# Optimization experiments

Measured on AMD Instinct MI355X. Metric: run time of the kernel, lower is better.

Reference implementation:

```python
import jax, jax.numpy as jnp
import numpy as np

B, T, C, H, HS, L, V = 16, 2048, 16, 2, 8, 2, 256
EPS = 1e-5


def _ln(x, g, b):
    m = jnp.mean(x, axis=-1, keepdims=True)
    v = jnp.mean((x - m) ** 2, axis=-1, keepdims=True)
    return (x - m) / jnp.sqrt(v + EPS) * g + b


def setup_inputs() -> dict:
    key = jax.random.key(0)
    ks = jax.random.split(key, 10)
    p = lambda k, s: (0.02 * jax.random.normal(k, s)).astype(jnp.float32)
    return {
        "idx": jax.random.randint(ks[0], (B, T), 0, V),
        "tok_emb": p(ks[1], (V, C)),          # tied with lm_head
        "pos_emb": p(ks[2], (T, C)),
        "wq": p(ks[3], (L, H, C, HS)),
        "wk": p(ks[4], (L, H, C, HS)),
        "wv": p(ks[5], (L, H, C, HS)),
        "wo": p(ks[6], (L, C, C)),            # torch Linear weight: (out, in)
        "ln1_g": jnp.ones((L, C), jnp.float32),
        "ln1_b": jnp.zeros((L, C), jnp.float32),
        "ln2_g": jnp.ones((L, C), jnp.float32),
        "ln2_b": jnp.zeros((L, C), jnp.float32),
        "w1": p(ks[7], (L, 4 * C, C)),
        "w2": p(ks[8], (L, C, 4 * C)),
        "lnf_g": jnp.ones((C,), jnp.float32),
        "lnf_b": jnp.zeros((C,), jnp.float32),
    }


def reference(idx, tok_emb, pos_emb, wq, wk, wv, wo, ln1_g, ln1_b,
              ln2_g, ln2_b, w1, w2, lnf_g, lnf_b):
    Tc = idx.shape[1]
    x = tok_emb[idx] + pos_emb[:Tc]                      # [B,T,C]
    causal = jnp.tril(jnp.ones((Tc, Tc), dtype=bool))
    scale = HS ** -0.5
    for l in range(L):
        h = _ln(x, ln1_g[l], ln1_b[l])
        q = jnp.einsum('btc,hcs->bhts', h, wq[l])
        k = jnp.einsum('btc,hcs->bhts', h, wk[l])
        v = jnp.einsum('btc,hcs->bhts', h, wv[l])
        scores = jnp.einsum('bhts,bhus->bhtu', q, k) * scale
        scores = jnp.where(causal, scores, -jnp.inf)
        attn = jax.nn.softmax(scores, axis=-1)           # [B,H,T,T]
        o = jnp.einsum('bhtu,bhus->bhts', attn, v)       # [B,H,T,HS]
        o = o.transpose(0, 2, 1, 3).reshape(x.shape[0], Tc, C)  # concat heads
        x = x + o @ wo[l].T
        h = _ln(x, ln2_g[l], ln2_b[l])
        x = x + jax.nn.relu(h @ w1[l].T) @ w2[l].T
    x = _ln(x, lnf_g, lnf_b)
    return x @ tok_emb.T                                 # tied lm_head: [B,T,V]
```

## Files before the change

kernel.cpp:

```cpp
#include <hip/hip_runtime.h>
#include <math.h>

constexpr int Bc  = 16;
constexpr int Tc  = 2048;
constexpr int Cc  = 16;
constexpr int Hc  = 2;
constexpr int HSc = 8;
constexpr int Vc  = 256;
constexpr int BT  = Bc * Tc;
constexpr float EPSc = 1e-5f;


typedef short s8v __attribute__((ext_vector_type(8)));
typedef float f4v __attribute__((ext_vector_type(4)));

constexpr int WS = 20;

__device__ inline float shx(float v, int m) { return __shfl_xor(v, m, 64); }

__device__ inline unsigned short f2bf(float f) {
  union { float f; unsigned u; } c; c.f = f;
  unsigned u = c.u + 0x7fffu + ((c.u >> 16) & 1u);
  return (unsigned short)(u >> 16);
}

__device__ inline unsigned cvtpk(float a, float b) {
  unsigned r;
  asm("v_cvt_pk_bf16_f32 %0, %1, %2" : "=v"(r) : "v"(a), "v"(b));
  return r;
}

__device__ inline void layernorm16(const float* xr, float* h,
                                   const float* g, const float* b) {
  float m = 0.f;
#pragma unroll
  for (int c = 0; c < Cc; c++) m += xr[c];
  m *= (1.f / Cc);
  float var = 0.f;
#pragma unroll
  for (int c = 0; c < Cc; c++) { float d = xr[c] - m; var += d * d; }
  var *= (1.f / Cc);
  float rs = rsqrtf(var + EPSc);
#pragma unroll
  for (int c = 0; c < Cc; c++) h[c] = (xr[c] - m) * rs * g[c] + b[c];
}

__device__ inline void qkv_store_bf16(const float* h, const float* swq,
                                      const float* swk, const float* swv,
                                      int bb, int tt, int j,
                                      unsigned short* __restrict__ qb,
                                      unsigned short* __restrict__ kb,
                                      unsigned short* sv) {
  const float pre = 0.35355339059327373f * 1.4426950408889634f;
  int a = tt & 31;
  int col = (tt & 32) | ((((a & 15) >> 2)) << 3) | (((a >> 4) & 1) << 2) |
            (a & 3);
#pragma unroll
  for (int hh = 0; hh < Hc; hh++) {
    float q0 = 0.f, q1 = 0.f, k0 = 0.f, k1 = 0.f, v0 = 0.f, v1 = 0.f;
#pragma unroll
    for (int c = 0; c < Cc; c++) {
      float hv = h[c];
      const float* wqp = swq + (hh * Cc + c) * HSc + 2 * j;
      const float* wkp = swk + (hh * Cc + c) * HSc + 2 * j;
      const float* wvp = swv + (hh * Cc + c) * HSc + 2 * j;
      q0 += hv * wqp[0]; q1 += hv * wqp[1];
      k0 += hv * wkp[0]; k1 += hv * wkp[1];
      v0 += hv * wvp[0]; v1 += hv * wvp[1];
    }
    int bh = bb * Hc + hh;
    long rowb = ((long)bh * Tc + tt) * 8 + 2 * j;
    unsigned qp = (unsigned)f2bf(q0 * pre) | ((unsigned)f2bf(q1 * pre) << 16);
    unsigned kp = (unsigned)f2bf(k0) | ((unsigned)f2bf(k1) << 16);
    *(unsigned*)(qb + rowb) = qp;
    *(unsigned*)(kb + rowb) = kp;
    sv[(hh * 8 + 2 * j) * 64 + col]     = f2bf(v0);
    sv[(hh * 8 + 2 * j + 1) * 64 + col] = f2bf(v1);
  }
}

__device__ inline void vt_writeout(const unsigned short* sv, int bb, int t0,
                                   int tid, unsigned short* __restrict__ vt) {
  int r  = tid >> 4;
  int cs = (tid & 15) * 4;
  int bh = bb * Hc + (r >> 3);
  int d  = r & 7;
  *(uint2*)(vt + ((long)bh * 8 + d) * Tc + t0 + cs) =
      *(const uint2*)(sv + r * 64 + cs);
}

__global__ __launch_bounds__(256, 4) void embed_ln_qkv_kernel(
    const int* __restrict__ idx, const float* __restrict__ tok,
    const float* __restrict__ pos,
    const float* __restrict__ wq, const float* __restrict__ wk,
    const float* __restrict__ wv,
    const float* __restrict__ g, const float* __restrict__ b,
    float* __restrict__ x, unsigned short* __restrict__ qb,
    unsigned short* __restrict__ kb, unsigned short* __restrict__ vt,
    unsigned short* __restrict__ zp) {
  __shared__ float swq[256], swk[256], swv[256], sg[Cc], sb[Cc];
  __shared__ unsigned short sv[16 * 64];
  int tid = threadIdx.x;
  if (blockIdx.x == 0 && tid < 16) ((unsigned*)zp)[tid] = 0u;
  swq[tid] = wq[tid];
  swk[tid] = wk[tid];
  swv[tid] = wv[tid];
  if (tid < Cc) { sg[tid] = g[tid]; sb[tid] = b[tid]; }
  __syncthreads();

  int tk = blockIdx.x * 64 + (tid >> 2);
  int j  = tid & 3;
  int tt = tk & (Tc - 1);
  int bb = tk >> 11;
  int id = idx[tk];
  float xr[Cc];
  const float4* te = (const float4*)(tok + id * Cc);
  const float4* pe = (const float4*)(pos + tt * Cc);
#pragma unroll
  for (int i = 0; i < 4; i++) {
    float4 a = te[i], p = pe[i];
    xr[4*i] = a.x + p.x; xr[4*i+1] = a.y + p.y;
    xr[4*i+2] = a.z + p.z; xr[4*i+3] = a.w + p.w;
  }
  ((float4*)(x + (long)tk * Cc))[j] =
      make_float4(xr[4*j], xr[4*j+1], xr[4*j+2], xr[4*j+3]);
  float h[Cc];
  layernorm16(xr, h, sg, sb);
  qkv_store_bf16(h, swq, swk, swv, bb, tt, j, qb, kb, sv);
  __syncthreads();
  vt_writeout(sv, bb, (blockIdx.x * 64) & (Tc - 1), tid, vt);
}

__device__ inline void attn_wave(const unsigned short* __restrict__ qb,
                                 const unsigned short* __restrict__ kb,
                                 const unsigned short* __restrict__ vt,
                                 const unsigned short* __restrict__ zp,
                                 int bh, int pairId, int lane, int wv_,
                                 float* so) {
  int lq = lane & 15;
  int g4 = (lane >> 4) << 2;
  bool real16 = lane < 16;
  bool real8  = lq < 8;
  bool md[4];
#pragma unroll
  for (int r = 0; r < 4; r++) md[r] = (g4 + r) <= lq;

  const f4v zf = {0.f, 0.f, 0.f, 0.f};

#pragma unroll 1
  for (int hf = 0; hf < 2; hf++) {
    int qt = hf ? (127 - pairId) : pairId;
    int q0 = qt << 4;
    int NB = (qt + 2) >> 1;

    s8v qf = *(real16 ? (const s8v*)(qb + ((long)bh * Tc + q0 + lq) * 8)
                      : (const s8v*)zp);
    const unsigned short* kp_ = real16 ? kb + ((long)bh * Tc + lq) * 8 : zp;
    long kts = real16 ? 128 : 0;
    const unsigned short* vp_ =
        real8 ? vt + ((long)bh * 8 + lq) * Tc + (g4 << 1) : zp;
    long vts = real8 ? 32 : 0;

    f4v oacc = zf;
    float lsum = 0.f;

    s8v kf0 = *(const s8v*)kp_;
    s8v kf1 = *(const s8v*)(kp_ + kts);
    kp_ += 2 * kts;
    s8v vf = *(const s8v*)vp_;
    vp_ += vts;

    for (int b = 0; b < NB - 1; b++) {
      s8v kn0 = *(const s8v*)kp_;
      s8v kn1 = *(const s8v*)(kp_ + kts);
      kp_ += 2 * kts;
      s8v vn = *(const s8v*)vp_;
      vp_ += vts;

      f4v st0 = __builtin_amdgcn_mfma_f32_16x16x32_bf16(kf0, qf, zf, 0, 0, 0);
      f4v st1 = __builtin_amdgcn_mfma_f32_16x16x32_bf16(kf1, qf, zf, 0, 0, 0);
      float p00 = __builtin_amdgcn_exp2f(st0[0]);
      float p01 = __builtin_amdgcn_exp2f(st0[1]);
      float p02 = __builtin_amdgcn_exp2f(st0[2]);
      float p03 = __builtin_amdgcn_exp2f(st0[3]);
      float p10 = __builtin_amdgcn_exp2f(st1[0]);
      float p11 = __builtin_amdgcn_exp2f(st1[1]);
      float p12 = __builtin_amdgcn_exp2f(st1[2]);
      float p13 = __builtin_amdgcn_exp2f(st1[3]);
      lsum += ((p00 + p01) + (p02 + p03)) + ((p10 + p11) + (p12 + p13));
      union { unsigned u[4]; s8v s; } pu;
      pu.u[0] = cvtpk(p00, p01);
      pu.u[1] = cvtpk(p02, p03);
      pu.u[2] = cvtpk(p10, p11);
      pu.u[3] = cvtpk(p12, p13);
      oacc = __builtin_amdgcn_mfma_f32_16x16x32_bf16(pu.s, vf, oacc, 0, 0, 0);
      kf0 = kn0; kf1 = kn1; vf = vn;
    }

    {
      f4v st0 = __builtin_amdgcn_mfma_f32_16x16x32_bf16(kf0, qf, zf, 0, 0, 0);
      float p0[4], p1[4];
#pragma unroll
      for (int r = 0; r < 4; r++) p0[r] = __builtin_amdgcn_exp2f(st0[r]);
      if (qt & 1) {
        f4v st1 =
            __builtin_amdgcn_mfma_f32_16x16x32_bf16(kf1, qf, zf, 0, 0, 0);
#pragma unroll
        for (int r = 0; r < 4; r++) {
          float e = __builtin_amdgcn_exp2f(st1[r]);
          p1[r] = md[r] ? e : 0.f;
        }
      } else {
#pragma unroll
        for (int r = 0; r < 4; r++) {
          p0[r] = md[r] ? p0[r] : 0.f;
          p1[r] = 0.f;
        }
      }
      lsum += ((p0[0] + p0[1]) + (p0[2] + p0[3])) +
              ((p1[0] + p1[1]) + (p1[2] + p1[3]));
      union { unsigned u[4]; s8v s; } pu;
      pu.u[0] = cvtpk(p0[0], p0[1]);
      pu.u[1] = cvtpk(p0[2], p0[3]);
      pu.u[2] = cvtpk(p1[0], p1[1]);
      pu.u[3] = cvtpk(p1[2], p1[3]);
      oacc = __builtin_amdgcn_mfma_f32_16x16x32_bf16(pu.s, vf, oacc, 0, 0, 0);
    }

    lsum += shx(lsum, 16);
    lsum += shx(lsum, 32);
    float inv = 1.0f / lsum;
    float invr[4];
#pragma unroll
    for (int r = 0; r < 4; r++) invr[r] = __shfl(inv, g4 + r, 64);
    if (real8) {
      float* ob = so + (hf * 16 + g4) * WS + wv_ * 8 + lq;
#pragma unroll
      for (int r = 0; r < 4; r++) ob[r * WS] = oacc[r] * invr[r];
    }
  }
}

__device__ inline void tail_core(
    const float* so, const float* swo, const float* sw1, const float* sw2t,
    const float* sg2, const float* sb2, int tl, int j, float* xr) {
  float orow[Cc];
  {
    const float4* op = (const float4*)(so + tl * WS);
    float4 a = op[0], b = op[1], c = op[2], d = op[3];
    orow[0]=a.x; orow[1]=a.y; orow[2]=a.z; orow[3]=a.w;
    orow[4]=b.x; orow[5]=b.y; orow[6]=b.z; orow[7]=b.w;
    orow[8]=c.x; orow[9]=c.y; orow[10]=c.z; orow[11]=c.w;
    orow[12]=d.x; orow[13]=d.y; orow[14]=d.z; orow[15]=d.w;
  }
  float xc[4];
#pragma unroll
  for (int qq = 0; qq < 4; qq++) {
    int c = 4 * j + qq;
    const float4* wr = (const float4*)(swo + c * WS);
    float4 wa = wr[0], wb = wr[1], wc = wr[2], wd = wr[3];
    float acc = xr[c]
      + orow[0]*wa.x + orow[1]*wa.y + orow[2]*wa.z + orow[3]*wa.w
      + orow[4]*wb.x + orow[5]*wb.y + orow[6]*wb.z + orow[7]*wb.w
      + orow[8]*wc.x + orow[9]*wc.y + orow[10]*wc.z + orow[11]*wc.w
      + orow[12]*wd.x + orow[13]*wd.y + orow[14]*wd.z + orow[15]*wd.w;
    xc[qq] = acc;
  }
  {
    float p[4];
#pragma unroll
    for (int qq = 0; qq < 4; qq++) p[qq] = shx(xc[qq], 1);
    bool lo = (j & 1) == 0;
    float a8[8], b8[8];
#pragma unroll
    for (int qq = 0; qq < 4; qq++) {
      a8[qq]     = lo ? xc[qq] : p[qq];
      a8[4 + qq] = lo ? p[qq] : xc[qq];
    }
#pragma unroll
    for (int s = 0; s < 8; s++) b8[s] = shx(a8[s], 2);
    bool lo2 = (j & 2) == 0;
#pragma unroll
    for (int s = 0; s < 8; s++) {
      xr[s]     = lo2 ? a8[s] : b8[s];
      xr[8 + s] = lo2 ? b8[s] : a8[s];
    }
  }
  float h[Cc];
  layernorm16(xr, h, sg2, sb2);
  float r[Cc];
#pragma unroll
  for (int c = 0; c < Cc; c++) r[c] = 0.f;
#pragma unroll
  for (int i = 0; i < 16; i++) {
    int jj = i * 4 + j;
    const float4* w1r = (const float4*)(sw1 + jj * WS);
    float4 wa = w1r[0], wb = w1r[1], wc = w1r[2], wd = w1r[3];
    float acc =
        h[0]*wa.x + h[1]*wa.y + h[2]*wa.z + h[3]*wa.w
      + h[4]*wb.x + h[5]*wb.y + h[6]*wb.z + h[7]*wb.w
      + h[8]*wc.x + h[9]*wc.y + h[10]*wc.z + h[11]*wc.w
      + h[12]*wd.x + h[13]*wd.y + h[14]*wd.z + h[15]*wd.w;
    acc = fmaxf(acc, 0.f);
    const float4* w2r = (const float4*)(sw2t + jj * WS);
    float4 va = w2r[0], vb = w2r[1], vc = w2r[2], vd = w2r[3];
    r[0]+=acc*va.x;  r[1]+=acc*va.y;  r[2]+=acc*va.z;  r[3]+=acc*va.w;
    r[4]+=acc*vb.x;  r[5]+=acc*vb.y;  r[6]+=acc*vb.z;  r[7]+=acc*vb.w;
    r[8]+=acc*vc.x;  r[9]+=acc*vc.y;  r[10]+=acc*vc.z; r[11]+=acc*vc.w;
    r[12]+=acc*vd.x; r[13]+=acc*vd.y; r[14]+=acc*vd.z; r[15]+=acc*vd.w;
  }
#pragma unroll
  for (int c = 0; c < Cc; c++) r[c] += shx(r[c], 1);
#pragma unroll
  for (int c = 0; c < Cc; c++) r[c] += shx(r[c], 2);
#pragma unroll
  for (int c = 0; c < Cc; c++) xr[c] += r[c];
}

__global__ __launch_bounds__(128, 2) void attn_mid_kernel(
    const unsigned short* __restrict__ qb0,
    const unsigned short* __restrict__ kb0,
    const unsigned short* __restrict__ vt0,
    const unsigned short* __restrict__ zp,
    const float* __restrict__ wo, const float* __restrict__ g2,
    const float* __restrict__ b2, const float* __restrict__ w1,
    const float* __restrict__ w2,
    const float* __restrict__ wq, const float* __restrict__ wk,
    const float* __restrict__ wv, const float* __restrict__ g1,
    const float* __restrict__ b1,
    float* __restrict__ x, unsigned short* __restrict__ qb1,
    unsigned short* __restrict__ kb1, unsigned short* __restrict__ vt1) {
  __shared__ float swo[16 * WS], sw1[64 * WS], sw2t[64 * WS];
  __shared__ float swq[256], swk[256], swv[256];
  __shared__ float sg2[Cc], sb2[Cc], sg1[Cc], sb1[Cc];
  __shared__ float so[32 * WS];
  __shared__ unsigned short sv[2 * 16 * 16];
  int tid = threadIdx.x;
  for (int t = tid; t < 256; t += 128) {
    swq[t] = wq[t]; swk[t] = wk[t]; swv[t] = wv[t];
    swo[(t >> 4) * WS + (t & 15)] = wo[t];
  }
  for (int t = tid; t < 1024; t += 128) {
    sw1[(t >> 4) * WS + (t & 15)] = w1[t];
    sw2t[(t & 63) * WS + (t >> 6)] = w2[t];
  }
  if (tid < Cc) {
    sg2[tid] = g2[tid]; sb2[tid] = b2[tid];
    sg1[tid] = g1[tid]; sb1[tid] = b1[tid];
  }
  __syncthreads();

  int b  = blockIdx.x & 15;
  int p  = blockIdx.x >> 4;
  int wv_ = tid >> 6, lane = tid & 63;
  attn_wave(qb0, kb0, vt0, zp, b * Hc + wv_, p, lane, wv_, so);
  __syncthreads();

  int tl = tid >> 2, j = tid & 3;
  int qtT = (tl < 16) ? p : (127 - p);
  int tt  = qtT * 16 + (tl & 15);
  long tk = (long)b * Tc + tt;
  float xr[Cc];
  {
    const float4* xp = (const float4*)(x + tk * Cc);
#pragma unroll
    for (int i = 0; i < 4; i++) {
      float4 a = xp[i];
      xr[4*i]=a.x; xr[4*i+1]=a.y; xr[4*i+2]=a.z; xr[4*i+3]=a.w;
    }
  }
  tail_core(so, swo, sw1, sw2t, sg2, sb2, tl, j, xr);
  ((float4*)(x + tk * Cc))[j] =
      make_float4(xr[4*j], xr[4*j+1], xr[4*j+2], xr[4*j+3]);
  float h[Cc];
  layernorm16(xr, h, sg1, sb1);
  {
    const float pre = 0.35355339059327373f * 1.4426950408889634f;
    int i  = tt & 15;
    int cd = 4 * (i >> 2) + (i & 3);
    int tau = tl >> 4;
#pragma unroll
    for (int hh = 0; hh < Hc; hh++) {
      float q0 = 0.f, q1 = 0.f, k0 = 0.f, k1 = 0.f, v0 = 0.f, v1 = 0.f;
#pragma unroll
      for (int c = 0; c < Cc; c++) {
        float hv = h[c];
        const float* wqp = swq + (hh * Cc + c) * HSc + 2 * j;
        const float* wkp = swk + (hh * Cc + c) * HSc + 2 * j;
        const float* wvp = swv + (hh * Cc + c) * HSc + 2 * j;
        q0 += hv * wqp[0]; q1 += hv * wqp[1];
        k0 += hv * wkp[0]; k1 += hv * wkp[1];
        v0 += hv * wvp[0]; v1 += hv * wvp[1];
      }
      int bh = b * Hc + hh;
      long rowb = ((long)bh * Tc + tt) * 8 + 2 * j;
      *(unsigned*)(qb1 + rowb) =
          (unsigned)f2bf(q0 * pre) | ((unsigned)f2bf(q1 * pre) << 16);
      *(unsigned*)(kb1 + rowb) =
          (unsigned)f2bf(k0) | ((unsigned)f2bf(k1) << 16);
      sv[(tau * 16 + hh * 8 + 2 * j) * 16 + cd]     = f2bf(v0);
      sv[(tau * 16 + hh * 8 + 2 * j + 1) * 16 + cd] = f2bf(v1);
    }
  }
  __syncthreads();
  {
    int tau = tid >> 6, rr = (tid >> 2) & 15, G = tid & 3;
    int qt_ = tau ? (127 - p) : p;
    int bh  = b * Hc + (rr >> 3), d = rr & 7;
    int gcol = ((qt_ & ~1) << 4) + 8 * G + 4 * (qt_ & 1);
    *(uint2*)(vt1 + ((long)bh * 8 + d) * Tc + gcol) =
        *(const uint2*)(sv + (tau * 16 + rr) * 16 + 4 * G);
  }
}

__global__ __launch_bounds__(128, 2) void attn_lnf_head_kernel(
    const unsigned short* __restrict__ qb1,
    const unsigned short* __restrict__ kb1,
    const unsigned short* __restrict__ vt1,
    const unsigned short* __restrict__ zp,
    const float* __restrict__ wo, const float* __restrict__ g2,
    const float* __restrict__ b2, const float* __restrict__ w1,
    const float* __restrict__ w2, const float* __restrict__ gf,
    const float* __restrict__ bf,
    float* __restrict__ x, const float* __restrict__ tok,
    float* __restrict__ out) {
  __shared__ float swo[16 * WS], sw1[64 * WS], sw2t[64 * WS];
  __shared__ float sg2[Cc], sb2[Cc], sgf[Cc], sbf[Cc];
  __shared__ float so[32 * WS];
  __shared__ float shf[32 * WS];
  int tid = threadIdx.x;
  for (int t = tid; t < 256; t += 128) {
    swo[(t >> 4) * WS + (t & 15)] = wo[t];
  }
  for (int t = tid; t < 1024; t += 128) {
    sw1[(t >> 4) * WS + (t & 15)] = w1[t];
    sw2t[(t & 63) * WS + (t >> 6)] = w2[t];
  }
  if (tid < Cc) {
    sg2[tid] = g2[tid]; sb2[tid] = b2[tid];
    sgf[tid] = gf[tid]; sbf[tid] = bf[tid];
  }
  __syncthreads();

  int b  = blockIdx.x & 15;
  int p  = blockIdx.x >> 4;
  int wv_ = tid >> 6, lane = tid & 63;
  attn_wave(qb1, kb1, vt1, zp, b * Hc + wv_, p, lane, wv_, so);
  __syncthreads();

  int tl = tid >> 2, j = tid & 3;
  int qtT = (tl < 16) ? p : (127 - p);
  int tt  = qtT * 16 + (tl & 15);
  long tk = (long)b * Tc + tt;
  float xr[Cc];
  {
    const float4* xp = (const float4*)(x + tk * Cc);
#pragma unroll
    for (int i = 0; i < 4; i++) {
      float4 a = xp[i];
      xr[4*i]=a.x; xr[4*i+1]=a.y; xr[4*i+2]=a.z; xr[4*i+3]=a.w;
    }
  }
  tail_core(so, swo, sw1, sw2t, sg2, sb2, tl, j, xr);
  float h[Cc];
  layernorm16(xr, h, sgf, sbf);
  *(float4*)(shf + tl * WS + 4 * j) =
      make_float4(h[4*j], h[4*j+1], h[4*j+2], h[4*j+3]);
  __syncthreads();

  float4 e0a, e1a, e2a, e3a, e0b, e1b, e2b, e3b;
  {
    const float4* ea = (const float4*)(tok + tid * Cc);
    e0a = ea[0]; e1a = ea[1]; e2a = ea[2]; e3a = ea[3];
    const float4* eb = (const float4*)(tok + (tid + 128) * Cc);
    e0b = eb[0]; e1b = eb[1]; e2b = eb[2]; e3b = eb[3];
  }
#pragma unroll 4
  for (int t = 0; t < 32; t++) {
    const float4* hp = (const float4*)(shf + t * WS);
    float4 h0 = hp[0], h1 = hp[1], h2 = hp[2], h3 = hp[3];
    float a0 = h0.x*e0a.x + h0.y*e0a.y + h0.z*e0a.z + h0.w*e0a.w
             + h1.x*e1a.x + h1.y*e1a.y + h1.z*e1a.z + h1.w*e1a.w
             + h2.x*e2a.x + h2.y*e2a.y + h2.z*e2a.z + h2.w*e2a.w
             + h3.x*e3a.x + h3.y*e3a.y + h3.z*e3a.z + h3.w*e3a.w;
    float a1 = h0.x*e0b.x + h0.y*e0b.y + h0.z*e0b.z + h0.w*e0b.w
             + h1.x*e1b.x + h1.y*e1b.y + h1.z*e1b.z + h1.w*e1b.w
             + h2.x*e2b.x + h2.y*e2b.y + h2.z*e2b.z + h2.w*e2b.w
             + h3.x*e3b.x + h3.y*e3b.y + h3.z*e3b.z + h3.w*e3b.w;
    int qtH = (t < 16) ? p : (127 - p);
    long row = ((long)b * Tc + qtH * 16 + (t & 15)) * Vc;
    out[row + tid]       = a0;
    out[row + tid + 128] = a1;
  }
}

extern "C" void kernel_launch(void* const* d_in, const int* in_sizes, int n_in,
                              void* d_out, int out_size, void* d_ws,
                              size_t ws_size, hipStream_t stream) {
  const int*   idx  = (const int*)  d_in[0];
  const float* tok  = (const float*)d_in[1];
  const float* pos  = (const float*)d_in[2];
  const float* wq   = (const float*)d_in[3];
  const float* wk   = (const float*)d_in[4];
  const float* wv   = (const float*)d_in[5];
  const float* wo   = (const float*)d_in[6];
  const float* ln1g = (const float*)d_in[7];
  const float* ln1b = (const float*)d_in[8];
  const float* ln2g = (const float*)d_in[9];
  const float* ln2b = (const float*)d_in[10];
  const float* w1   = (const float*)d_in[11];
  const float* w2   = (const float*)d_in[12];
  const float* lnfg = (const float*)d_in[13];
  const float* lnfb = (const float*)d_in[14];
  float* out = (float*)d_out;

  float* x = (float*)d_ws;
  unsigned short* qb0 = (unsigned short*)(x + (long)BT * Cc);
  unsigned short* kb0 = qb0 + (long)Bc * Hc * Tc * HSc;
  unsigned short* vt0 = kb0 + (long)Bc * Hc * Tc * HSc;
  unsigned short* qb1 = vt0 + (long)Bc * Hc * Tc * HSc;
  unsigned short* kb1 = qb1 + (long)Bc * Hc * Tc * HSc;
  unsigned short* vt1 = kb1 + (long)Bc * Hc * Tc * HSc;
  unsigned short* zp  = vt1 + (long)Bc * Hc * Tc * HSc;

  embed_ln_qkv_kernel<<<BT / 64, 256, 0, stream>>>(
      idx, tok, pos, wq, wk, wv, ln1g, ln1b, x, qb0, kb0, vt0, zp);
  attn_mid_kernel<<<1024, 128, 0, stream>>>(
      qb0, kb0, vt0, zp, wo, ln2g, ln2b, w1, w2,
      wq + Hc * Cc * HSc, wk + Hc * Cc * HSc, wv + Hc * Cc * HSc,
      ln1g + Cc, ln1b + Cc, x, qb1, kb1, vt1);
  attn_lnf_head_kernel<<<1024, 128, 0, stream>>>(
      qb1, kb1, vt1, zp, wo + Cc * Cc, ln2g + Cc, ln2b + Cc,
      w1 + 4 * Cc * Cc, w2 + 4 * Cc * Cc, lnfg, lnfb, x, tok, out);
}
```

Baseline: 163.1 us.

## Split attention query-tile halves across four waves per block

Each attention block now launches 256 threads (4 waves) instead of 128. Each wave handles one head and one of the two paired query tiles, where before one wave looped over both tiles in sequence. This doubles wave-level parallelism and shortens the per-wave serial critical path. The MLP tail runs on only half the threads, leaving two waves idle there, while the LM-head projection uses all 256 threads with one vocab column each.

```diff
diff --git a/kernel.cpp b/kernel.cpp
--- a/kernel.cpp
+++ b/kernel.cpp
@@ -135,7 +135,7 @@
                                  const unsigned short* __restrict__ kb,
                                  const unsigned short* __restrict__ vt,
                                  const unsigned short* __restrict__ zp,
-                                 int bh, int pairId, int lane, int wv_,
+                                 int bh, int qt, int lane, int hd, int hf,
                                  float* so) {
   int lq = lane & 15;
   int g4 = (lane >> 4) << 2;
@@ -147,97 +147,92 @@
 
   const f4v zf = {0.f, 0.f, 0.f, 0.f};
 
-#pragma unroll 1
-  for (int hf = 0; hf < 2; hf++) {
-    int qt = hf ? (127 - pairId) : pairId;
-    int q0 = qt << 4;
-    int NB = (qt + 2) >> 1;
-
-    s8v qf = *(real16 ? (const s8v*)(qb + ((long)bh * Tc + q0 + lq) * 8)
-                      : (const s8v*)zp);
-    const unsigned short* kp_ = real16 ? kb + ((long)bh * Tc + lq) * 8 : zp;
-    long kts = real16 ? 128 : 0;
-    const unsigned short* vp_ =
-        real8 ? vt + ((long)bh * 8 + lq) * Tc + (g4 << 1) : zp;
-    long vts = real8 ? 32 : 0;
-
-    f4v oacc = zf;
-    float lsum = 0.f;
-
-    s8v kf0 = *(const s8v*)kp_;
-    s8v kf1 = *(const s8v*)(kp_ + kts);
+  int q0 = qt << 4;
+  int NB = (qt + 2) >> 1;
+
+  s8v qf = *(real16 ? (const s8v*)(qb + ((long)bh * Tc + q0 + lq) * 8)
+                    : (const s8v*)zp);
+  const unsigned short* kp_ = real16 ? kb + ((long)bh * Tc + lq) * 8 : zp;
+  long kts = real16 ? 128 : 0;
+  const unsigned short* vp_ =
+      real8 ? vt + ((long)bh * 8 + lq) * Tc + (g4 << 1) : zp;
+  long vts = real8 ? 32 : 0;
+
+  f4v oacc = zf;
+  float lsum = 0.f;
+
+  s8v kf0 = *(const s8v*)kp_;
+  s8v kf1 = *(const s8v*)(kp_ + kts);
+  kp_ += 2 * kts;
+  s8v vf = *(const s8v*)vp_;
+  vp_ += vts;
+
+  for (int b = 0; b < NB - 1; b++) {
+    s8v kn0 = *(const s8v*)kp_;
+    s8v kn1 = *(const s8v*)(kp_ + kts);
     kp_ += 2 * kts;
-    s8v vf = *(const s8v*)vp_;
+    s8v vn = *(const s8v*)vp_;
     vp_ += vts;
 
-    for (int b = 0; b < NB - 1; b++) {
-      s8v kn0 = *(const s8v*)kp_;
-      s8v kn1 = *(const s8v*)(kp_ + kts);
-      kp_ += 2 * kts;
-      s8v vn = *(const s8v*)vp_;
-      vp_ += vts;
-
-      f4v st0 = __builtin_amdgcn_mfma_f32_16x16x32_bf16(kf0, qf, zf, 0, 0, 0);
+    f4v st0 = __builtin_amdgcn_mfma_f32_16x16x32_bf16(kf0, qf, zf, 0, 0, 0);
+    f4v st1 = __builtin_amdgcn_mfma_f32_16x16x32_bf16(kf1, qf, zf, 0, 0, 0);
+    float p00 = __builtin_amdgcn_exp2f(st0[0]);
+    float p01 = __builtin_amdgcn_exp2f(st0[1]);
+    float p02 = __builtin_amdgcn_exp2f(st0[2]);
+    float p03 = __builtin_amdgcn_exp2f(st0[3]);
+    float p10 = __builtin_amdgcn_exp2f(st1[0]);
+    float p11 = __builtin_amdgcn_exp2f(st1[1]);
+    float p12 = __builtin_amdgcn_exp2f(st1[2]);
+    float p13 = __builtin_amdgcn_exp2f(st1[3]);
+    lsum += ((p00 + p01) + (p02 + p03)) + ((p10 + p11) + (p12 + p13));
+    union { unsigned u[4]; s8v s; } pu;
+    pu.u[0] = cvtpk(p00, p01);
+    pu.u[1] = cvtpk(p02, p03);
+    pu.u[2] = cvtpk(p10, p11);
+    pu.u[3] = cvtpk(p12, p13);
+    oacc = __builtin_amdgcn_mfma_f32_16x16x32_bf16(pu.s, vf, oacc, 0, 0, 0);
+    kf0 = kn0; kf1 = kn1; vf = vn;
+  }
+
+  {
+    f4v st0 = __builtin_amdgcn_mfma_f32_16x16x32_bf16(kf0, qf, zf, 0, 0, 0);
+    float p0[4], p1[4];
+#pragma unroll
+    for (int r = 0; r < 4; r++) p0[r] = __builtin_amdgcn_exp2f(st0[r]);
+    if (qt & 1) {
       f4v st1 = __builtin_amdgcn_mfma_f32_16x16x32_bf16(kf1, qf, zf, 0, 0, 0);
-      float p00 = __builtin_amdgcn_exp2f(st0[0]);
-      float p01 = __builtin_amdgcn_exp2f(st0[1]);
-      float p02 = __builtin_amdgcn_exp2f(st0[2]);
-      float p03 = __builtin_amdgcn_exp2f(st0[3]);
-      float p10 = __builtin_amdgcn_exp2f(st1[0]);
-      float p11 = __builtin_amdgcn_exp2f(st1[1]);
-      float p12 = __builtin_amdgcn_exp2f(st1[2]);
-      float p13 = __builtin_amdgcn_exp2f(st1[3]);
-      lsum += ((p00 + p01) + (p02 + p03)) + ((p10 + p11) + (p12 + p13));
-      union { unsigned u[4]; s8v s; } pu;
-      pu.u[0] = cvtpk(p00, p01);
-      pu.u[1] = cvtpk(p02, p03);
-      pu.u[2] = cvtpk(p10, p11);
-      pu.u[3] = cvtpk(p12, p13);
-      oacc = __builtin_amdgcn_mfma_f32_16x16x32_bf16(pu.s, vf, oacc, 0, 0, 0);
-      kf0 = kn0; kf1 = kn1; vf = vn;
-    }
-
-    {
-      f4v st0 = __builtin_amdgcn_mfma_f32_16x16x32_bf16(kf0, qf, zf, 0, 0, 0);
-      float p0[4], p1[4];
-#pragma unroll
-      for (int r = 0; r < 4; r++) p0[r] = __builtin_amdgcn_exp2f(st0[r]);
-      if (qt & 1) {
-        f4v st1 =
-            __builtin_amdgcn_mfma_f32_16x16x32_bf16(kf1, qf, zf, 0, 0, 0);
-#pragma unroll
-        for (int r = 0; r < 4; r++) {
-          float e = __builtin_amdgcn_exp2f(st1[r]);
-          p1[r] = md[r] ? e : 0.f;
-        }
-      } else {
-#pragma unroll
-        for (int r = 0; r < 4; r++) {
-          p0[r] = md[r] ? p0[r] : 0.f;
-          p1[r] = 0.f;
-        }
+#pragma unroll
+      for (int r = 0; r < 4; r++) {
+        float e = __builtin_amdgcn_exp2f(st1[r]);
+        p1[r] = md[r] ? e : 0.f;
       }
-      lsum += ((p0[0] + p0[1]) + (p0[2] + p0[3])) +
-              ((p1[0] + p1[1]) + (p1[2] + p1[3]));
-      union { unsigned u[4]; s8v s; } pu;
-      pu.u[0] = cvtpk(p0[0], p0[1]);
-      pu.u[1] = cvtpk(p0[2], p0[3]);
-      pu.u[2] = cvtpk(p1[0], p1[1]);
-      pu.u[3] = cvtpk(p1[2], p1[3]);
-      oacc = __builtin_amdgcn_mfma_f32_16x16x32_bf16(pu.s, vf, oacc, 0, 0, 0);
-    }
-
-    lsum += shx(lsum, 16);
-    lsum += shx(lsum, 32);
-    float inv = 1.0f / lsum;
-    float invr[4];
-#pragma unroll
-    for (int r = 0; r < 4; r++) invr[r] = __shfl(inv, g4 + r, 64);
-    if (real8) {
-      float* ob = so + (hf * 16 + g4) * WS + wv_ * 8 + lq;
-#pragma unroll
-      for (int r = 0; r < 4; r++) ob[r * WS] = oacc[r] * invr[r];
-    }
+    } else {
+#pragma unroll
+      for (int r = 0; r < 4; r++) {
+        p0[r] = md[r] ? p0[r] : 0.f;
+        p1[r] = 0.f;
+      }
+    }
+    lsum += ((p0[0] + p0[1]) + (p0[2] + p0[3])) +
+            ((p1[0] + p1[1]) + (p1[2] + p1[3]));
+    union { unsigned u[4]; s8v s; } pu;
+    pu.u[0] = cvtpk(p0[0], p0[1]);
+    pu.u[1] = cvtpk(p0[2], p0[3]);
+    pu.u[2] = cvtpk(p1[0], p1[1]);
+    pu.u[3] = cvtpk(p1[2], p1[3]);
+    oacc = __builtin_amdgcn_mfma_f32_16x16x32_bf16(pu.s, vf, oacc, 0, 0, 0);
+  }
+
+  lsum += shx(lsum, 16);
+  lsum += shx(lsum, 32);
+  float inv = 1.0f / lsum;
+  float invr[4];
+#pragma unroll
+  for (int r = 0; r < 4; r++) invr[r] = __shfl(inv, g4 + r, 64);
+  if (real8) {
+    float* ob = so + (hf * 16 + g4) * WS + hd * 8 + lq;
+#pragma unroll
+    for (int r = 0; r < 4; r++) ob[r * WS] = oacc[r] * invr[r];
   }
 }
 
@@ -317,7 +312,7 @@
   for (int c = 0; c < Cc; c++) xr[c] += r[c];
 }
 
-__global__ __launch_bounds__(128, 2) void attn_mid_kernel(
+__global__ __launch_bounds__(256, 4) void attn_mid_kernel(
     const unsigned short* __restrict__ qb0,
     const unsigned short* __restrict__ kb0,
     const unsigned short* __restrict__ vt0,
@@ -336,11 +331,14 @@
   __shared__ float so[32 * WS];
   __shared__ unsigned short sv[2 * 16 * 16];
   int tid = threadIdx.x;
-  for (int t = tid; t < 256; t += 128) {
-    swq[t] = wq[t]; swk[t] = wk[t]; swv[t] = wv[t];
-    swo[(t >> 4) * WS + (t & 15)] = wo[t];
-  }
-  for (int t = tid; t < 1024; t += 128) {
+  {
+    int t = tid;
+    if (t < 256) {
+      swq[t] = wq[t]; swk[t] = wk[t]; swv[t] = wv[t];
+      swo[(t >> 4) * WS + (t & 15)] = wo[t];
+    }
+  }
+  for (int t = tid; t < 1024; t += 256) {
     sw1[(t >> 4) * WS + (t & 15)] = w1[t];
     sw2t[(t & 63) * WS + (t >> 6)] = w2[t];
   }
@@ -352,29 +350,31 @@
 
   int b  = blockIdx.x & 15;
   int p  = blockIdx.x >> 4;
-  int wv_ = tid >> 6, lane = tid & 63;
-  attn_wave(qb0, kb0, vt0, zp, b * Hc + wv_, p, lane, wv_, so);
-  __syncthreads();
-
-  int tl = tid >> 2, j = tid & 3;
-  int qtT = (tl < 16) ? p : (127 - p);
-  int tt  = qtT * 16 + (tl & 15);
-  long tk = (long)b * Tc + tt;
-  float xr[Cc];
-  {
-    const float4* xp = (const float4*)(x + tk * Cc);
-#pragma unroll
-    for (int i = 0; i < 4; i++) {
-      float4 a = xp[i];
-      xr[4*i]=a.x; xr[4*i+1]=a.y; xr[4*i+2]=a.z; xr[4*i+3]=a.w;
-    }
-  }
-  tail_core(so, swo, sw1, sw2t, sg2, sb2, tl, j, xr);
-  ((float4*)(x + tk * Cc))[j] =
-      make_float4(xr[4*j], xr[4*j+1], xr[4*j+2], xr[4*j+3]);
-  float h[Cc];
-  layernorm16(xr, h, sg1, sb1);
-  {
+  int w  = tid >> 6, lane = tid & 63;
+  int hd = w & 1, hf = w >> 1;
+  int qtw = hf ? (127 - p) : p;
+  attn_wave(qb0, kb0, vt0, zp, b * Hc + hd, qtw, lane, hd, hf, so);
+  __syncthreads();
+
+  if (tid < 128) {
+    int tl = tid >> 2, j = tid & 3;
+    int qtT = (tl < 16) ? p : (127 - p);
+    int tt  = qtT * 16 + (tl & 15);
+    long tk = (long)b * Tc + tt;
+    float xr[Cc];
+    {
+      const float4* xp = (const float4*)(x + tk * Cc);
+#pragma unroll
+      for (int i = 0; i < 4; i++) {
+        float4 a = xp[i];
+        xr[4*i]=a.x; xr[4*i+1]=a.y; xr[4*i+2]=a.z; xr[4*i+3]=a.w;
+      }
+    }
+    tail_core(so, swo, sw1, sw2t, sg2, sb2, tl, j, xr);
+    ((float4*)(x + tk * Cc))[j] =
+        make_float4(xr[4*j], xr[4*j+1], xr[4*j+2], xr[4*j+3]);
+    float h[Cc];
+    layernorm16(xr, h, sg1, sb1);
     const float pre = 0.35355339059327373f * 1.4426950408889634f;
     int i  = tt & 15;
     int cd = 4 * (i >> 2) + (i & 3);
@@ -403,7 +403,7 @@
     }
   }
   __syncthreads();
-  {
+  if (tid < 128) {
     int tau = tid >> 6, rr = (tid >> 2) & 15, G = tid & 3;
     int qt_ = tau ? (127 - p) : p;
     int bh  = b * Hc + (rr >> 3), d = rr & 7;
@@ -413,7 +413,7 @@
   }
 }
 
-__global__ __launch_bounds__(128, 2) void attn_lnf_head_kernel(
+__global__ __launch_bounds__(256, 4) void attn_lnf_head_kernel(
     const unsigned short* __restrict__ qb1,
     const unsigned short* __restrict__ kb1,
     const unsigned short* __restrict__ vt1,
@@ -429,10 +429,10 @@
   __shared__ float so[32 * WS];
   __shared__ float shf[32 * WS];
   int tid = threadIdx.x;
-  for (int t = tid; t < 256; t += 128) {
-    swo[(t >> 4) * WS + (t & 15)] = wo[t];
-  }
-  for (int t = tid; t < 1024; t += 128) {
+  if (tid < 256) {
+    swo[(tid >> 4) * WS + (tid & 15)] = wo[tid];
+  }
+  for (int t = tid; t < 1024; t += 256) {
     sw1[(t >> 4) * WS + (t & 15)] = w1[t];
     sw2t[(t & 63) * WS + (t >> 6)] = w2[t];
   }
@@ -444,53 +444,50 @@
 
   int b  = blockIdx.x & 15;
   int p  = blockIdx.x >> 4;
-  int wv_ = tid >> 6, lane = tid & 63;
-  attn_wave(qb1, kb1, vt1, zp, b * Hc + wv_, p, lane, wv_, so);
-  __syncthreads();
-
-  int tl = tid >> 2, j = tid & 3;
-  int qtT = (tl < 16) ? p : (127 - p);
-  int tt  = qtT * 16 + (tl & 15);
-  long tk = (long)b * Tc + tt;
-  float xr[Cc];
+  int w  = tid >> 6, lane = tid & 63;
+  int hd = w & 1, hf = w >> 1;
+  int qtw = hf ? (127 - p) : p;
+  attn_wave(qb1, kb1, vt1, zp, b * Hc + hd, qtw, lane, hd, hf, so);
+  __syncthreads();
+
+  if (tid < 128) {
+    int tl = tid >> 2, j = tid & 3;
+    int qtT = (tl < 16) ? p : (127 - p);
+    int tt  = qtT * 16 + (tl & 15);
+    long tk = (long)b * Tc + tt;
+    float xr[Cc];
+    {
+      const float4* xp = (const float4*)(x + tk * Cc);
+#pragma unroll
+      for (int i = 0; i < 4; i++) {
+        float4 a = xp[i];
+        xr[4*i]=a.x; xr[4*i+1]=a.y; xr[4*i+2]=a.z; xr[4*i+3]=a.w;
+      }
+    }
+    tail_core(so, swo, sw1, sw2t, sg2, sb2, tl, j, xr);
+    float h[Cc];
+    layernorm16(xr, h, sgf, sbf);
+    *(float4*)(shf + tl * WS + 4 * j) =
+        make_float4(h[4*j], h[4*j+1], h[4*j+2], h[4*j+3]);
+  }
+  __syncthreads();
+
+  float4 e0, e1, e2, e3;
   {
-    const float4* xp = (const float4*)(x + tk * Cc);
-#pragma unroll
-    for (int i = 0; i < 4; i++) {
-      float4 a = xp[i];
-      xr[4*i]=a.x; xr[4*i+1]=a.y; xr[4*i+2]=a.z; xr[4*i+3]=a.w;
-    }
-  }
-  tail_core(so, swo, sw1, sw2t, sg2, sb2, tl, j, xr);
-  float h[Cc];
-  layernorm16(xr, h, sgf, sbf);
-  *(float4*)(shf + tl * WS + 4 * j) =
-      make_float4(h[4*j], h[4*j+1], h[4*j+2], h[4*j+3]);
-  __syncthreads();
-
-  float4 e0a, e1a, e2a, e3a, e0b, e1b, e2b, e3b;
-  {
-    const float4* ea = (const float4*)(tok + tid * Cc);
-    e0a = ea[0]; e1a = ea[1]; e2a = ea[2]; e3a = ea[3];
-    const float4* eb = (const float4*)(tok + (tid + 128) * Cc);
-    e0b = eb[0]; e1b = eb[1]; e2b = eb[2]; e3b = eb[3];
+    const float4* ep = (const float4*)(tok + tid * Cc);
+    e0 = ep[0]; e1 = ep[1]; e2 = ep[2]; e3 = ep[3];
   }
 #pragma unroll 4
   for (int t = 0; t < 32; t++) {
     const float4* hp = (const float4*)(shf + t * WS);
     float4 h0 = hp[0], h1 = hp[1], h2 = hp[2], h3 = hp[3];
-    float a0 = h0.x*e0a.x + h0.y*e0a.y + h0.z*e0a.z + h0.w*e0a.w
-             + h1.x*e1a.x + h1.y*e1a.y + h1.z*e1a.z + h1.w*e1a.w
-             + h2.x*e2a.x + h2.y*e2a.y + h2.z*e2a.z + h2.w*e2a.w
-             + h3.x*e3a.x + h3.y*e3a.y + h3.z*e3a.z + h3.w*e3a.w;
-    float a1 = h0.x*e0b.x + h0.y*e0b.y + h0.z*e0b.z + h0.w*e0b.w
-             + h1.x*e1b.x + h1.y*e1b.y + h1.z*e1b.z + h1.w*e1b.w
-             + h2.x*e2b.x + h2.y*e2b.y + h2.z*e2b.z + h2.w*e2b.w
-             + h3.x*e3b.x + h3.y*e3b.y + h3.z*e3b.z + h3.w*e3b.w;
+    float a0 = h0.x*e0.x + h0.y*e0.y + h0.z*e0.z + h0.w*e0.w
+             + h1.x*e1.x + h1.y*e1.y + h1.z*e1.z + h1.w*e1.w
+             + h2.x*e2.x + h2.y*e2.y + h2.z*e2.z + h2.w*e2.w
+             + h3.x*e3.x + h3.y*e3.y + h3.z*e3.z + h3.w*e3.w;
     int qtH = (t < 16) ? p : (127 - p);
     long row = ((long)b * Tc + qtH * 16 + (t & 15)) * Vc;
-    out[row + tid]       = a0;
-    out[row + tid + 128] = a1;
+    out[row + tid] = a0;
   }
 }
 
@@ -525,11 +522,11 @@
 
   embed_ln_qkv_kernel<<<BT / 64, 256, 0, stream>>>(
       idx, tok, pos, wq, wk, wv, ln1g, ln1b, x, qb0, kb0, vt0, zp);
-  attn_mid_kernel<<<1024, 128, 0, stream>>>(
+  attn_mid_kernel<<<1024, 256, 0, stream>>>(
       qb0, kb0, vt0, zp, wo, ln2g, ln2b, w1, w2,
       wq + Hc * Cc * HSc, wk + Hc * Cc * HSc, wv + Hc * Cc * HSc,
       ln1g + Cc, ln1b + Cc, x, qb1, kb1, vt1);
-  attn_lnf_head_kernel<<<1024, 128, 0, stream>>>(
+  attn_lnf_head_kernel<<<1024, 256, 0, stream>>>(
       qb1, kb1, vt1, zp, wo + Cc * Cc, ln2g + Cc, ln2b + Cc,
       w1 + 4 * Cc * Cc, w2 + 4 * Cc * Cc, lnfg, lnfb, x, tok, out);
 }
```

After: 156.7 us (median of 2 runs). 3.9% less time.
